# Kernel optimization log

Hardware: AMD Instinct MI355X
Metric: run time of the kernel (lower is better)

Reference implementation:

```python
import jax, jax.numpy as jnp
import numpy as np


def setup_inputs() -> dict:
    key = jax.random.key(0)
    x = jax.random.normal(key, (32, 3, 512, 512), dtype=jnp.float32)
    return {"x": x}


def reference(x):
    # Faithful vectorized form of the triple-loop 2x2 block flatten:
    # out[b, c*H*W + i*W + 4*j + 2*r + s] = x[b, c, 2*i + r, 2*j + s]
    B, C, H, W = x.shape
    # [B, C, H//2, 2, W//2, 2] -> (b, c, i, r, j, s)
    y = x.reshape(B, C, H // 2, 2, W // 2, 2)
    # reorder to (b, c, i, j, r, s); flattening (i, j, r, s) yields
    # i*(W//2*4) + j*4 + r*2 + s = i*W + 4*j + 2*r + s, matching the loop offsets
    y = jnp.transpose(y, (0, 1, 2, 4, 3, 5))
    return y.reshape(B, C * H * W)
```

## Files before the change

kernel.cpp:

```cpp
#include <hip/hip_runtime.h>


namespace {
constexpr int B = 32;
constexpr int C = 3;
constexpr int H = 512;
constexpr int W = 512;
constexpr int TILE_FLOATS = 4096;
constexpr int NTILES = B * C * H * W / TILE_FLOATS;
}

__global__ __launch_bounds__(256) void flatten2x2_lds(const float* __restrict__ x,
                                                      float* __restrict__ out) {
    __shared__ float lds[TILE_FLOATS];

    const int tid = threadIdx.x;
    const int w = tid >> 6;
    const int lane = tid & 63;

    const long long tile = (long long)blockIdx.x * TILE_FLOATS;

    const float4* __restrict__ src = (const float4*)(x + tile + 1024 * w);
    float4* ldsv = (float4*)(lds + 1024 * w);
#pragma unroll
    for (int m = 0; m < 4; ++m) {
        ldsv[64 * m + lane] = src[64 * m + lane];
    }
    __syncthreads();

    const float2* r0 = (const float2*)(lds + 1024 * w);
    const float2* r1 = (const float2*)(lds + 1024 * w + 512);
    float4* __restrict__ dst = (float4*)(out + tile + 1024 * w);
#pragma unroll
    for (int m = 0; m < 4; ++m) {
        const int j = 64 * m + lane;
        const float2 a = r0[j];
        const float2 b = r1[j];
        dst[j] = make_float4(a.x, a.y, b.x, b.y);
    }
}

extern "C" void kernel_launch(void* const* d_in, const int* in_sizes, int n_in,
                              void* d_out, int out_size, void* d_ws, size_t ws_size,
                              hipStream_t stream) {
    const float* x = (const float*)d_in[0];
    float* out = (float*)d_out;

    flatten2x2_lds<<<NTILES, 256, 0, stream>>>(x, out);
}
```

Baseline: 174.8 us.

## Replace LDS staging with direct float2 loads, deep unroll, nontemporal stores

Drops the shared-memory tile and barrier. Each thread now loads two float2 values straight from global memory, one from each of the paired rows, and writes a float4 with a nontemporal store. The grid shrinks to 1536 blocks, and each block runs two iterations of 8 unrolled chunks per wave so more loads are in flight. The trade-off is narrower 8-byte loads instead of 16-byte ones and lower block-level parallelism.

```diff
diff --git a/kernel.cpp b/kernel.cpp
--- a/kernel.cpp
+++ b/kernel.cpp
@@ -2,41 +2,41 @@
 
 
 namespace {
-constexpr int B = 32;
-constexpr int C = 3;
-constexpr int H = 512;
-constexpr int W = 512;
-constexpr int TILE_FLOATS = 4096;
-constexpr int NTILES = B * C * H * W / TILE_FLOATS;
+constexpr int UNROLL = 8;
+constexpr int BLOCKS = 1536;
+constexpr int ITERS  = 2;
 }
 
-__global__ __launch_bounds__(256) void flatten2x2_lds(const float* __restrict__ x,
-                                                      float* __restrict__ out) {
-    __shared__ float lds[TILE_FLOATS];
+typedef float fx2 __attribute__((ext_vector_type(2)));
+typedef float fx4 __attribute__((ext_vector_type(4)));
 
-    const int tid = threadIdx.x;
-    const int w = tid >> 6;
+__global__ __launch_bounds__(256) void flatten2x2_deep(const float* __restrict__ x,
+                                                       float* __restrict__ out) {
+    const int tid  = (int)threadIdx.x;
+    const int w    = tid >> 6;
     const int lane = tid & 63;
 
-    const long long tile = (long long)blockIdx.x * TILE_FLOATS;
+    const fx2* __restrict__ x2 = (const fx2*)x;
+    fx4* __restrict__ o4       = (fx4*)out;
 
-    const float4* __restrict__ src = (const float4*)(x + tile + 1024 * w);
-    float4* ldsv = (float4*)(lds + 1024 * w);
+    for (int it = 0; it < ITERS; ++it) {
+        const int chunk0 = ((int)blockIdx.x * ITERS + it) * (4 * UNROLL) + w * UNROLL;
+
+        fx2 a[UNROLL], b[UNROLL];
 #pragma unroll
-    for (int m = 0; m < 4; ++m) {
-        ldsv[64 * m + lane] = src[64 * m + lane];
-    }
-    __syncthreads();
-
-    const float2* r0 = (const float2*)(lds + 1024 * w);
-    const float2* r1 = (const float2*)(lds + 1024 * w + 512);
-    float4* __restrict__ dst = (float4*)(out + tile + 1024 * w);
+        for (int u = 0; u < UNROLL; ++u) {
+            const int g  = (chunk0 + u) * 64 + lane;
+            const int f2 = g + ((g >> 8) << 8);
+            a[u] = x2[f2];
+            b[u] = x2[f2 + 256];
+        }
 #pragma unroll
-    for (int m = 0; m < 4; ++m) {
-        const int j = 64 * m + lane;
-        const float2 a = r0[j];
-        const float2 b = r1[j];
-        dst[j] = make_float4(a.x, a.y, b.x, b.y);
+        for (int u = 0; u < UNROLL; ++u) {
+            const int g = (chunk0 + u) * 64 + lane;
+            fx4 v;
+            v.x = a[u].x; v.y = a[u].y; v.z = b[u].x; v.w = b[u].y;
+            __builtin_nontemporal_store(v, &o4[g]);
+        }
     }
 }
 
@@ -45,6 +45,5 @@
                               hipStream_t stream) {
     const float* x = (const float*)d_in[0];
     float* out = (float*)d_out;
-
-    flatten2x2_lds<<<NTILES, 256, 0, stream>>>(x, out);
+    flatten2x2_deep<<<BLOCKS, 256, 0, stream>>>(x, out);
 }
```

Measured after the change: 178.5 us. +2.2%, slower.
